# Kernel optimization log

Hardware: AMD Instinct MI355X
Metric: run time of the kernel (lower is better)

The kernel has to match this reference:

```python
import jax, jax.numpy as jnp
import numpy as np

B, CATT, D, H, W = 4, 8, 48, 128, 256
CF, EMB, HEADS, WIN = 80, 64, 4, 3
WIN2 = WIN * WIN
HEAD_DIM = EMB // HEADS
SCALE = HEAD_DIM ** -0.5


def setup_inputs() -> dict:
    key = jax.random.key(0)
    ks = jax.random.split(key, 7)
    attn_vol = jax.random.normal(ks[0], (B, CATT, D, H, W), dtype=jnp.float32)
    feat_map = jax.random.normal(ks[1], (B, CF, H, W), dtype=jnp.float32)
    # disp_gap in [0,4) so roughly half the pixels satisfy (disp_gap >= 2)
    disp_gap = jax.random.uniform(ks[2], (B, 1, H, W), dtype=jnp.float32) * 4.0
    xav = (6.0 / (EMB + CF)) ** 0.5
    Wq = jax.random.uniform(ks[3], (EMB, CF), jnp.float32, -xav, xav)
    Wk = jax.random.uniform(ks[4], (EMB, CF), jnp.float32, -xav, xav)
    Wv = jax.random.uniform(ks[5], (EMB, CF), jnp.float32, -xav, xav)
    # out_proj weight is zero-initialized in the module; use small random for a
    # non-degenerate correctness baseline
    Wo = jax.random.normal(ks[6], (CATT, EMB), dtype=jnp.float32) * 0.02
    return {"attn_vol": attn_vol, "feat_map": feat_map, "disp_gap": disp_gap,
            "Wq": Wq, "Wk": Wk, "Wv": Wv, "Wo": Wo}


def _unfold3x3_torch_layout(x):
    # x: (B, E, H, W) -> (B, N, WIN2, E) matching torch's
    # unfold(...).transpose(1,2).view(B, N, win2, emb), where unfold channel
    # index is c*9 + w (channel-major). The subsequent view therefore MIXES
    # channels and window positions; we reproduce that exactly.
    b, e, h, w = x.shape
    p = WIN // 2
    xp = jnp.pad(x, ((0, 0), (0, 0), (p, p), (p, p)))
    pat = jnp.stack([xp[:, :, i:i + h, j:j + w]
                     for i in range(WIN) for j in range(WIN)], axis=2)  # (B,E,9,H,W)
    pat = pat.reshape(b, e * WIN2, h * w)          # torch unfold layout c*9+w
    pat = pat.transpose(0, 2, 1)                   # (B, N, E*9)
    return pat.reshape(b, h * w, WIN2, e)          # faithful (mixed) view


def reference(attn_vol, feat_map, disp_gap, Wq, Wk, Wv, Wo):
    b, c_att, d, h, w = attn_vol.shape
    n = h * w
    Q = jnp.einsum('bchw,ec->behw', feat_map, Wq)
    K = jnp.einsum('bchw,ec->behw', feat_map, Wk)
    V = jnp.einsum('bchw,ec->behw', feat_map, Wv)

    Ku = _unfold3x3_torch_layout(K)  # (B, N, 9, EMB)
    Vu = _unfold3x3_torch_layout(V)

    # split heads
    Qh = Q.reshape(b, EMB, n).transpose(0, 2, 1)
    Qh = Qh.reshape(b, n, HEADS, HEAD_DIM).transpose(0, 2, 1, 3)          # (B,h,N,hd)
    Kh = Ku.reshape(b, n, WIN2, HEADS, HEAD_DIM).transpose(0, 3, 1, 2, 4)  # (B,h,N,9,hd)
    Vh = Vu.reshape(b, n, WIN2, HEADS, HEAD_DIM).transpose(0, 3, 1, 2, 4)

    scores = jnp.einsum('bhnd,bhnwd->bhnw', Qh, Kh) * SCALE
    probs = jax.nn.softmax(scores, axis=-1)
    ctx = jnp.einsum('bhnw,bhnwd->bhnd', probs, Vh)                        # (B,h,N,hd)

    ctx = ctx.transpose(0, 2, 1, 3).reshape(b, n, EMB)
    delta2d = ctx.transpose(0, 2, 1).reshape(b, EMB, h, w)
    delta2d = jnp.einsum('behw,ae->bahw', delta2d, Wo)                     # (B,CATT,H,W)

    mask = (disp_gap >= 2.0).reshape(b, 1, 1, h, w)
    delta = jnp.where(mask, 0.0, delta2d[:, :, None, :, :])               # (B,CATT,D,H,W)
    return attn_vol + delta
```

## Files before the change

### kernel.cpp

```cpp
#include <hip/hip_runtime.h>
#include <math.h>

namespace {
constexpr int Bc   = 4;
constexpr int CATT = 8;
constexpr int Dd   = 48;
constexpr int Hh   = 128;
constexpr int Ww   = 256;
constexpr int CF   = 80;
constexpr int EMB  = 64;
constexpr int HEADS = 4;
constexpr int Nn   = Hh * Ww;
constexpr float SCALE = 0.25f;

constexpr size_t WS_KV    = 0;
constexpr size_t WS_DELTA = (size_t)Bc * Nn * 128;
constexpr size_t WS_WTKV  = WS_DELTA + (size_t)Bc * CATT * Nn;
constexpr size_t WS_WTQ   = WS_WTKV + (size_t)CF * 128;
}

__global__ void prep_weights_k(const float* __restrict__ Wq,
                               const float* __restrict__ Wk,
                               const float* __restrict__ Wv,
                               float* __restrict__ wtkv,
                               float* __restrict__ wtq) {
  const int t = blockIdx.x * blockDim.x + threadIdx.x;
  const int stride = gridDim.x * blockDim.x;
  for (int i = t; i < CF * 128; i += stride) {
    const int c = i >> 7, o = i & 127;
    wtkv[i] = (o < 64) ? Wk[o * CF + c] : Wv[(o - 64) * CF + c];
  }
  for (int i = t; i < CF * 64; i += stride) {
    const int c = i >> 6, e = i & 63;
    wtq[i] = Wq[e * CF + c] * SCALE;
  }
}

__global__ __launch_bounds__(256) void qkv_k(const float* __restrict__ feat,
                                             const float* __restrict__ wtkv,
                                             float* __restrict__ kv) {
  __shared__ float lf[CF][64];
  const int b  = blockIdx.y;
  const int n0 = blockIdx.x * 64;
  const int t  = threadIdx.x;

  const float* fb = feat + (size_t)b * CF * Nn + n0;
  for (int i = t; i < CF * 64; i += 256) {
    const int c = i >> 6, p = i & 63;
    lf[c][p] = fb[(size_t)c * Nn + p];
  }
  __syncthreads();

  const int og = t >> 4;
  const int p4 = (t & 15) * 4;

  float acc[8][4];
#pragma unroll
  for (int o = 0; o < 8; ++o)
#pragma unroll
    for (int j = 0; j < 4; ++j) acc[o][j] = 0.f;

  for (int c = 0; c < CF; ++c) {
    const float4 fv = *(const float4*)&lf[c][p4];
    const float fa[4] = {fv.x, fv.y, fv.z, fv.w};
    const float4 wa = *(const float4*)&wtkv[c * 128 + og * 8];
    const float4 wb = *(const float4*)&wtkv[c * 128 + og * 8 + 4];
    const float wv8[8] = {wa.x, wa.y, wa.z, wa.w, wb.x, wb.y, wb.z, wb.w};
#pragma unroll
    for (int o = 0; o < 8; ++o)
#pragma unroll
      for (int j = 0; j < 4; ++j) acc[o][j] = fmaf(wv8[o], fa[j], acc[o][j]);
  }

  float* outb = kv + ((size_t)b * Nn + n0) * 128;
#pragma unroll
  for (int j = 0; j < 4; ++j) {
    const int p = p4 + j;
    const float4 s0 = make_float4(acc[0][j], acc[1][j], acc[2][j], acc[3][j]);
    const float4 s1 = make_float4(acc[4][j], acc[5][j], acc[6][j], acc[7][j]);
    *(float4*)&outb[(size_t)p * 128 + og * 8]     = s0;
    *(float4*)&outb[(size_t)p * 128 + og * 8 + 4] = s1;
  }
}

__global__ __launch_bounds__(256) void attn_k(const float* __restrict__ feat,
                                              const float* __restrict__ kvbuf,
                                              const float* __restrict__ wtq,
                                              const float* __restrict__ Wo,
                                              const float* __restrict__ disp,
                                              float* __restrict__ delta) {
  const int b = blockIdx.y;
  const int n = blockIdx.x * 256 + threadIdx.x;
  const int h = n >> 8;
  const int w = n & 255;

  float q[EMB];
#pragma unroll
  for (int e = 0; e < EMB; ++e) q[e] = 0.f;
  {
    const float* fb = feat + (size_t)b * CF * Nn + n;
    for (int c = 0; c < CF; ++c) {
      const float fv = fb[(size_t)c * Nn];
#pragma unroll
      for (int e = 0; e < EMB; ++e) q[e] = fmaf(wtq[c * EMB + e], fv, q[e]);
    }
  }

  const float* kvb = kvbuf + (size_t)b * Nn * 128;

  float sc[HEADS * 9];
#pragma unroll
  for (int i = 0; i < HEADS * 9; ++i) sc[i] = 0.f;

#pragma unroll
  for (int widx = 0; widx < 9; ++widx) {
    const int di = widx / 3 - 1, dj = widx % 3 - 1;
    const int hh = h + di, ww = w + dj;
    if (hh < 0 || hh >= Hh || ww < 0 || ww >= Ww) continue;
    const float4* kn = (const float4*)(kvb + (size_t)(hh * Ww + ww) * 128);
#pragma unroll
    for (int e4 = 0; e4 < 16; ++e4) {
      const float4 kk = kn[e4];
      const float ka[4] = {kk.x, kk.y, kk.z, kk.w};
#pragma unroll
      for (int j = 0; j < 4; ++j) {
        const int f  = (e4 * 4 + j) * 9 + widx;
        const int w2 = f >> 6;
        const int e2 = f & 63;
        sc[(e2 >> 4) * 9 + w2] = fmaf(q[e2], ka[j], sc[(e2 >> 4) * 9 + w2]);
      }
    }
  }

  float probs[HEADS * 9];
#pragma unroll
  for (int hd = 0; hd < HEADS; ++hd) {
    float m = sc[hd * 9];
#pragma unroll
    for (int w2 = 1; w2 < 9; ++w2) m = fmaxf(m, sc[hd * 9 + w2]);
    float s = 0.f;
#pragma unroll
    for (int w2 = 0; w2 < 9; ++w2) {
      const float ev = __expf(sc[hd * 9 + w2] - m);
      probs[hd * 9 + w2] = ev;
      s += ev;
    }
    const float inv = 1.f / s;
#pragma unroll
    for (int w2 = 0; w2 < 9; ++w2) probs[hd * 9 + w2] *= inv;
  }

  float ctx[EMB];
#pragma unroll
  for (int e = 0; e < EMB; ++e) ctx[e] = 0.f;
#pragma unroll
  for (int widx = 0; widx < 9; ++widx) {
    const int di = widx / 3 - 1, dj = widx % 3 - 1;
    const int hh = h + di, ww = w + dj;
    if (hh < 0 || hh >= Hh || ww < 0 || ww >= Ww) continue;
    const float4* vn = (const float4*)(kvb + (size_t)(hh * Ww + ww) * 128 + 64);
#pragma unroll
    for (int e4 = 0; e4 < 16; ++e4) {
      const float4 vv = vn[e4];
      const float va[4] = {vv.x, vv.y, vv.z, vv.w};
#pragma unroll
      for (int j = 0; j < 4; ++j) {
        const int f  = (e4 * 4 + j) * 9 + widx;
        const int w2 = f >> 6;
        const int e2 = f & 63;
        ctx[e2] = fmaf(probs[(e2 >> 4) * 9 + w2], va[j], ctx[e2]);
      }
    }
  }

  const bool zero = (disp[(size_t)b * Nn + n] >= 2.0f);
  float* dout = delta + (size_t)b * CATT * Nn + n;
#pragma unroll
  for (int a = 0; a < CATT; ++a) {
    float s = 0.f;
#pragma unroll
    for (int e = 0; e < EMB; ++e) s = fmaf(Wo[a * EMB + e], ctx[e], s);
    dout[(size_t)a * Nn] = zero ? 0.f : s;
  }
}

__global__ __launch_bounds__(256) void add_k(const float* __restrict__ av,
                                             const float* __restrict__ delta,
                                             float* __restrict__ out) {
  const unsigned i4 = blockIdx.x * 256u + threadIdx.x;
  const unsigned n4 = i4 & 8191u;
  const unsigned t2 = i4 >> 13;
  const unsigned bc = t2 / 48u;
  const float4 a  = ((const float4*)av)[i4];
  const float4 dl = ((const float4*)delta)[(size_t)bc * 8192u + n4];
  float4 r;
  r.x = a.x + dl.x;
  r.y = a.y + dl.y;
  r.z = a.z + dl.z;
  r.w = a.w + dl.w;
  ((float4*)out)[i4] = r;
}

extern "C" void kernel_launch(void* const* d_in, const int* in_sizes, int n_in,
                              void* d_out, int out_size, void* d_ws, size_t ws_size,
                              hipStream_t stream) {
  const float* attn_vol = (const float*)d_in[0];
  const float* feat     = (const float*)d_in[1];
  const float* disp     = (const float*)d_in[2];
  const float* Wq       = (const float*)d_in[3];
  const float* Wk       = (const float*)d_in[4];
  const float* Wv       = (const float*)d_in[5];
  const float* Wo       = (const float*)d_in[6];
  float* out            = (float*)d_out;

  float* ws    = (float*)d_ws;
  float* kv    = ws + WS_KV;
  float* delta = ws + WS_DELTA;
  float* wtkv  = ws + WS_WTKV;
  float* wtq   = ws + WS_WTQ;

  hipLaunchKernelGGL(prep_weights_k, dim3(40), dim3(256), 0, stream,
                     Wq, Wk, Wv, wtkv, wtq);
  hipLaunchKernelGGL(qkv_k, dim3(Nn / 64, Bc), dim3(256), 0, stream,
                     feat, wtkv, kv);
  hipLaunchKernelGGL(attn_k, dim3(Nn / 256, Bc), dim3(256), 0, stream,
                     feat, kv, wtq, Wo, disp, delta);
  const int nf4 = out_size / 4;
  hipLaunchKernelGGL(add_k, dim3(nf4 / 256), dim3(256), 0, stream,
                     attn_vol, delta, out);
}
```

Measured before the change: 529.6 us.

## Store Q/K/V in zero-padded channel-major planes and split attention per head

Q, K and V are now all computed in the projection kernel and written as channel-major planes with a zero halo. The halo removes bounds checks, and neighbour reads become coalesced across adjacent pixels. The attention kernel gives each head its own 64-thread group with far fewer registers per thread, then reduces the per-head output-projection partials through shared memory. The old path stays as a fallback when the workspace is too small. The padded layout needs more workspace, and the prep kernel must zero the halo on every call.

```diff
diff --git a/kernel.cpp b/kernel.cpp
--- a/kernel.cpp
+++ b/kernel.cpp
@@ -4,19 +4,215 @@
 namespace {
 constexpr int Bc   = 4;
 constexpr int CATT = 8;
-constexpr int Dd   = 48;
 constexpr int Hh   = 128;
 constexpr int Ww   = 256;
 constexpr int CF   = 80;
 constexpr int EMB  = 64;
-constexpr int HEADS = 4;
 constexpr int Nn   = Hh * Ww;
 constexpr float SCALE = 0.25f;
 
-constexpr size_t WS_KV    = 0;
-constexpr size_t WS_DELTA = (size_t)Bc * Nn * 128;
-constexpr size_t WS_WTKV  = WS_DELTA + (size_t)Bc * CATT * Nn;
-constexpr size_t WS_WTQ   = WS_WTKV + (size_t)CF * 128;
+constexpr int ROWP  = 264;
+constexpr int PLANE = 130 * ROWP;
+constexpr size_t WS_KVQ   = 0;
+constexpr size_t WS_DELTA = (size_t)Bc * 192 * PLANE;
+constexpr size_t WS_WT    = WS_DELTA + (size_t)Bc * CATT * Nn;
+constexpr size_t WS_WOT   = WS_WT + (size_t)CF * 192;
+constexpr size_t WS_END   = WS_WOT + 512;
+constexpr size_t NEED_BYTES = WS_END * 4;
+
+constexpr size_t OWS_KV    = 0;
+constexpr size_t OWS_DELTA = (size_t)Bc * Nn * 128;
+constexpr size_t OWS_WTKV  = OWS_DELTA + (size_t)Bc * CATT * Nn;
+constexpr size_t OWS_WTQ   = OWS_WTKV + (size_t)CF * 128;
+}
+
+
+__global__ void prep_new_k(const float* __restrict__ Wq,
+                           const float* __restrict__ Wk,
+                           const float* __restrict__ Wv,
+                           const float* __restrict__ Wo,
+                           float* __restrict__ wt,
+                           float* __restrict__ wot,
+                           float* __restrict__ kvq) {
+  const int t = blockIdx.x * blockDim.x + threadIdx.x;
+  const int stride = gridDim.x * blockDim.x;
+  for (int i = t; i < CF * 192; i += stride) {
+    const int c = i / 192, o = i % 192;
+    float v;
+    if (o < 64)       v = Wq[o * CF + c] * SCALE;
+    else if (o < 128) v = Wk[(o - 64) * CF + c];
+    else              v = Wv[(o - 128) * CF + c];
+    wt[i] = v;
+  }
+  for (int i = t; i < 512; i += stride) {
+    const int e = i >> 3, a = i & 7;
+    wot[i] = Wo[a * EMB + e];
+  }
+  const int HALO = 1552;
+  for (int i = t; i < Bc * 192 * HALO; i += stride) {
+    const int plane = i / HALO;
+    const int r = i % HALO;
+    int row, col;
+    if (r < 264)        { row = 0;   col = r; }
+    else if (r < 528)   { row = 129; col = r - 264; }
+    else {
+      const int rr = r - 528;
+      row = (rr >> 3) + 1;
+      const int c8 = rr & 7;
+      col = (c8 < 4) ? c8 : (260 + c8 - 4);
+    }
+    kvq[(size_t)plane * PLANE + row * ROWP + col] = 0.f;
+  }
+}
+
+__global__ __launch_bounds__(256) void qkv_new_k(const float* __restrict__ feat,
+                                                 const float* __restrict__ wt,
+                                                 float* __restrict__ kvq) {
+  __shared__ float lf[CF][64];
+  const int b  = blockIdx.y;
+  const int n0 = blockIdx.x * 64;
+  const int t  = threadIdx.x;
+
+  const float* fb = feat + (size_t)b * CF * Nn + n0;
+  for (int i = t; i < CF * 64; i += 256) {
+    const int c = i >> 6, p = i & 63;
+    lf[c][p] = fb[(size_t)c * Nn + p];
+  }
+  __syncthreads();
+
+  const int og = t >> 4;
+  const int p4 = (t & 15) * 4;
+
+  float acc[12][4];
+#pragma unroll
+  for (int o = 0; o < 12; ++o)
+#pragma unroll
+    for (int j = 0; j < 4; ++j) acc[o][j] = 0.f;
+
+  for (int c = 0; c < CF; ++c) {
+    const float4 fv = *(const float4*)&lf[c][p4];
+    const float fa[4] = {fv.x, fv.y, fv.z, fv.w};
+    const float4 w0 = *(const float4*)&wt[c * 192 + og * 12];
+    const float4 w1 = *(const float4*)&wt[c * 192 + og * 12 + 4];
+    const float4 w2 = *(const float4*)&wt[c * 192 + og * 12 + 8];
+    const float wv12[12] = {w0.x, w0.y, w0.z, w0.w, w1.x, w1.y, w1.z, w1.w,
+                            w2.x, w2.y, w2.z, w2.w};
+#pragma unroll
+    for (int o = 0; o < 12; ++o)
+#pragma unroll
+      for (int j = 0; j < 4; ++j) acc[o][j] = fmaf(wv12[o], fa[j], acc[o][j]);
+  }
+
+  const int h = n0 >> 8, w0c = n0 & 255;
+  float* bbase = kvq + (size_t)b * 192 * PLANE;
+  const int rowoff = (h + 1) * ROWP + (w0c + 4) + p4;
+#pragma unroll
+  for (int o = 0; o < 12; ++o) {
+    const int oo = og * 12 + o;
+    *(float4*)&bbase[(size_t)oo * PLANE + rowoff] =
+        make_float4(acc[o][0], acc[o][1], acc[o][2], acc[o][3]);
+  }
+}
+
+template <int HD>
+__device__ __forceinline__ void attn_core(const float* __restrict__ kb, int coff,
+                                          const float* __restrict__ lwot,
+                                          float* __restrict__ part) {
+  float q16[16];
+#pragma unroll
+  for (int i = 0; i < 16; ++i)
+    q16[i] = kb[(size_t)(HD * 16 + i) * PLANE + coff];
+
+  float sc[9];
+#pragma unroll
+  for (int w2 = 0; w2 < 9; ++w2) {
+    float s = 0.f;
+#pragma unroll
+    for (int i = 0; i < 16; ++i) {
+      const int f = w2 * 64 + HD * 16 + i;
+      const int e = f / 9, widx = f % 9;
+      const int D = (widx / 3 - 1) * ROWP + (widx % 3 - 1);
+      s = fmaf(q16[i], kb[(size_t)(64 + e) * PLANE + coff + D], s);
+    }
+    sc[w2] = s;
+  }
+
+  float m = sc[0];
+#pragma unroll
+  for (int w2 = 1; w2 < 9; ++w2) m = fmaxf(m, sc[w2]);
+  float probs[9], ssum = 0.f;
+#pragma unroll
+  for (int w2 = 0; w2 < 9; ++w2) {
+    probs[w2] = __expf(sc[w2] - m);
+    ssum += probs[w2];
+  }
+  const float inv = 1.f / ssum;
+#pragma unroll
+  for (int w2 = 0; w2 < 9; ++w2) probs[w2] *= inv;
+
+  float ctx[16];
+#pragma unroll
+  for (int i = 0; i < 16; ++i) {
+    float c = 0.f;
+#pragma unroll
+    for (int w2 = 0; w2 < 9; ++w2) {
+      const int f = w2 * 64 + HD * 16 + i;
+      const int e = f / 9, widx = f % 9;
+      const int D = (widx / 3 - 1) * ROWP + (widx % 3 - 1);
+      c = fmaf(probs[w2], kb[(size_t)(128 + e) * PLANE + coff + D], c);
+    }
+    ctx[i] = c;
+  }
+
+#pragma unroll
+  for (int a = 0; a < 8; ++a) {
+    float p = 0.f;
+#pragma unroll
+    for (int i = 0; i < 16; ++i)
+      p = fmaf(lwot[(HD * 16 + i) * 8 + a], ctx[i], p);
+    part[a] = p;
+  }
+}
+
+__global__ __launch_bounds__(256) void attn_new_k(const float* __restrict__ kvq,
+                                                  const float* __restrict__ wot,
+                                                  const float* __restrict__ disp,
+                                                  float* __restrict__ delta) {
+  __shared__ float lwot[512];
+  __shared__ float lpart[4 * 576];
+  const int b = blockIdx.y;
+  const int t = threadIdx.x;
+  for (int i = t; i < 512; i += 256) lwot[i] = wot[i];
+  __syncthreads();
+
+  const int hd = t >> 6, lane = t & 63;
+  const int n = blockIdx.x * 64 + lane;
+  const int h = n >> 8, w = n & 255;
+  const int coff = (h + 1) * ROWP + (w + 4);
+  const float* kb = kvq + (size_t)b * 192 * PLANE;
+
+  float part[8];
+  switch (hd) {
+    case 0: attn_core<0>(kb, coff, lwot, part); break;
+    case 1: attn_core<1>(kb, coff, lwot, part); break;
+    case 2: attn_core<2>(kb, coff, lwot, part); break;
+    default: attn_core<3>(kb, coff, lwot, part); break;
+  }
+#pragma unroll
+  for (int a = 0; a < 8; ++a) lpart[hd * 576 + lane * 9 + a] = part[a];
+  __syncthreads();
+
+  const int px = t & 63, ag = t >> 6;
+  const int nn = blockIdx.x * 64 + px;
+  const bool zero = disp[(size_t)b * Nn + nn] >= 2.0f;
+  float* dout = delta + (size_t)b * CATT * Nn + nn;
+#pragma unroll
+  for (int k = 0; k < 2; ++k) {
+    const int a = ag * 2 + k;
+    const float s = lpart[0 * 576 + px * 9 + a] + lpart[1 * 576 + px * 9 + a] +
+                    lpart[2 * 576 + px * 9 + a] + lpart[3 * 576 + px * 9 + a];
+    dout[(size_t)a * Nn] = zero ? 0.f : s;
+  }
 }
 
 __global__ void prep_weights_k(const float* __restrict__ Wq,
@@ -43,23 +239,19 @@
   const int b  = blockIdx.y;
   const int n0 = blockIdx.x * 64;
   const int t  = threadIdx.x;
-
   const float* fb = feat + (size_t)b * CF * Nn + n0;
   for (int i = t; i < CF * 64; i += 256) {
     const int c = i >> 6, p = i & 63;
     lf[c][p] = fb[(size_t)c * Nn + p];
   }
   __syncthreads();
-
   const int og = t >> 4;
   const int p4 = (t & 15) * 4;
-
   float acc[8][4];
 #pragma unroll
   for (int o = 0; o < 8; ++o)
 #pragma unroll
     for (int j = 0; j < 4; ++j) acc[o][j] = 0.f;
-
   for (int c = 0; c < CF; ++c) {
     const float4 fv = *(const float4*)&lf[c][p4];
     const float fa[4] = {fv.x, fv.y, fv.z, fv.w};
@@ -71,15 +263,14 @@
 #pragma unroll
       for (int j = 0; j < 4; ++j) acc[o][j] = fmaf(wv8[o], fa[j], acc[o][j]);
   }
-
   float* outb = kv + ((size_t)b * Nn + n0) * 128;
 #pragma unroll
   for (int j = 0; j < 4; ++j) {
     const int p = p4 + j;
-    const float4 s0 = make_float4(acc[0][j], acc[1][j], acc[2][j], acc[3][j]);
-    const float4 s1 = make_float4(acc[4][j], acc[5][j], acc[6][j], acc[7][j]);
-    *(float4*)&outb[(size_t)p * 128 + og * 8]     = s0;
-    *(float4*)&outb[(size_t)p * 128 + og * 8 + 4] = s1;
+    *(float4*)&outb[(size_t)p * 128 + og * 8] =
+        make_float4(acc[0][j], acc[1][j], acc[2][j], acc[3][j]);
+    *(float4*)&outb[(size_t)p * 128 + og * 8 + 4] =
+        make_float4(acc[4][j], acc[5][j], acc[6][j], acc[7][j]);
   }
 }
 
@@ -93,7 +284,6 @@
   const int n = blockIdx.x * 256 + threadIdx.x;
   const int h = n >> 8;
   const int w = n & 255;
-
   float q[EMB];
 #pragma unroll
   for (int e = 0; e < EMB; ++e) q[e] = 0.f;
@@ -105,13 +295,10 @@
       for (int e = 0; e < EMB; ++e) q[e] = fmaf(wtq[c * EMB + e], fv, q[e]);
     }
   }
-
   const float* kvb = kvbuf + (size_t)b * Nn * 128;
-
-  float sc[HEADS * 9];
-#pragma unroll
-  for (int i = 0; i < HEADS * 9; ++i) sc[i] = 0.f;
-
+  float sc[36];
+#pragma unroll
+  for (int i = 0; i < 36; ++i) sc[i] = 0.f;
 #pragma unroll
   for (int widx = 0; widx < 9; ++widx) {
     const int di = widx / 3 - 1, dj = widx % 3 - 1;
@@ -124,32 +311,29 @@
       const float ka[4] = {kk.x, kk.y, kk.z, kk.w};
 #pragma unroll
       for (int j = 0; j < 4; ++j) {
-        const int f  = (e4 * 4 + j) * 9 + widx;
-        const int w2 = f >> 6;
-        const int e2 = f & 63;
+        const int f = (e4 * 4 + j) * 9 + widx;
+        const int w2 = f >> 6, e2 = f & 63;
         sc[(e2 >> 4) * 9 + w2] = fmaf(q[e2], ka[j], sc[(e2 >> 4) * 9 + w2]);
       }
     }
   }
-
-  float probs[HEADS * 9];
-#pragma unroll
-  for (int hd = 0; hd < HEADS; ++hd) {
-    float m = sc[hd * 9];
-#pragma unroll
-    for (int w2 = 1; w2 < 9; ++w2) m = fmaxf(m, sc[hd * 9 + w2]);
+  float probs[36];
+#pragma unroll
+  for (int hdx = 0; hdx < 4; ++hdx) {
+    float m = sc[hdx * 9];
+#pragma unroll
+    for (int w2 = 1; w2 < 9; ++w2) m = fmaxf(m, sc[hdx * 9 + w2]);
     float s = 0.f;
 #pragma unroll
     for (int w2 = 0; w2 < 9; ++w2) {
-      const float ev = __expf(sc[hd * 9 + w2] - m);
-      probs[hd * 9 + w2] = ev;
+      const float ev = __expf(sc[hdx * 9 + w2] - m);
+      probs[hdx * 9 + w2] = ev;
       s += ev;
     }
     const float inv = 1.f / s;
 #pragma unroll
-    for (int w2 = 0; w2 < 9; ++w2) probs[hd * 9 + w2] *= inv;
-  }
-
+    for (int w2 = 0; w2 < 9; ++w2) probs[hdx * 9 + w2] *= inv;
+  }
   float ctx[EMB];
 #pragma unroll
   for (int e = 0; e < EMB; ++e) ctx[e] = 0.f;
@@ -165,14 +349,12 @@
       const float va[4] = {vv.x, vv.y, vv.z, vv.w};
 #pragma unroll
       for (int j = 0; j < 4; ++j) {
-        const int f  = (e4 * 4 + j) * 9 + widx;
-        const int w2 = f >> 6;
-        const int e2 = f & 63;
+        const int f = (e4 * 4 + j) * 9 + widx;
+        const int w2 = f >> 6, e2 = f & 63;
         ctx[e2] = fmaf(probs[(e2 >> 4) * 9 + w2], va[j], ctx[e2]);
       }
     }
   }
-
   const bool zero = (disp[(size_t)b * Nn + n] >= 2.0f);
   float* dout = delta + (size_t)b * CATT * Nn + n;
 #pragma unroll
@@ -193,12 +375,7 @@
   const unsigned bc = t2 / 48u;
   const float4 a  = ((const float4*)av)[i4];
   const float4 dl = ((const float4*)delta)[(size_t)bc * 8192u + n4];
-  float4 r;
-  r.x = a.x + dl.x;
-  r.y = a.y + dl.y;
-  r.z = a.z + dl.z;
-  r.w = a.w + dl.w;
-  ((float4*)out)[i4] = r;
+  ((float4*)out)[i4] = make_float4(a.x + dl.x, a.y + dl.y, a.z + dl.z, a.w + dl.w);
 }
 
 extern "C" void kernel_launch(void* const* d_in, const int* in_sizes, int n_in,
@@ -212,20 +389,34 @@
   const float* Wv       = (const float*)d_in[5];
   const float* Wo       = (const float*)d_in[6];
   float* out            = (float*)d_out;
-
-  float* ws    = (float*)d_ws;
-  float* kv    = ws + WS_KV;
-  float* delta = ws + WS_DELTA;
-  float* wtkv  = ws + WS_WTKV;
-  float* wtq   = ws + WS_WTQ;
-
-  hipLaunchKernelGGL(prep_weights_k, dim3(40), dim3(256), 0, stream,
-                     Wq, Wk, Wv, wtkv, wtq);
-  hipLaunchKernelGGL(qkv_k, dim3(Nn / 64, Bc), dim3(256), 0, stream,
-                     feat, wtkv, kv);
-  hipLaunchKernelGGL(attn_k, dim3(Nn / 256, Bc), dim3(256), 0, stream,
-                     feat, kv, wtq, Wo, disp, delta);
+  float* ws             = (float*)d_ws;
   const int nf4 = out_size / 4;
-  hipLaunchKernelGGL(add_k, dim3(nf4 / 256), dim3(256), 0, stream,
-                     attn_vol, delta, out);
-}
+
+  if (ws_size >= NEED_BYTES) {
+    float* kvq   = ws + WS_KVQ;
+    float* delta = ws + WS_DELTA;
+    float* wt    = ws + WS_WT;
+    float* wot   = ws + WS_WOT;
+    hipLaunchKernelGGL(prep_new_k, dim3(512), dim3(256), 0, stream,
+                       Wq, Wk, Wv, Wo, wt, wot, kvq);
+    hipLaunchKernelGGL(qkv_new_k, dim3(Nn / 64, Bc), dim3(256), 0, stream,
+                       feat, wt, kvq);
+    hipLaunchKernelGGL(attn_new_k, dim3(Nn / 64, Bc), dim3(256), 0, stream,
+                       kvq, wot, disp, delta);
+    hipLaunchKernelGGL(add_k, dim3(nf4 / 256), dim3(256), 0, stream,
+                       attn_vol, delta, out);
+  } else {
+    float* kv    = ws + OWS_KV;
+    float* delta = ws + OWS_DELTA;
+    float* wtkv  = ws + OWS_WTKV;
+    float* wtq   = ws + OWS_WTQ;
+    hipLaunchKernelGGL(prep_weights_k, dim3(40), dim3(256), 0, stream,
+                       Wq, Wk, Wv, wtkv, wtq);
+    hipLaunchKernelGGL(qkv_k, dim3(Nn / 64, Bc), dim3(256), 0, stream,
+                       feat, wtkv, kv);
+    hipLaunchKernelGGL(attn_k, dim3(Nn / 256, Bc), dim3(256), 0, stream,
+                       feat, kv, wtq, Wo, disp, delta);
+    hipLaunchKernelGGL(add_k, dim3(nf4 / 256), dim3(256), 0, stream,
+                       attn_vol, delta, out);
+  }
+}
```

New measurement: 488.8 us. -7.7%, faster.
